# Performance work log

Hardware: AMD Instinct MI355X
Metric: run time of the kernel (lower is better)

The kernel has to match this reference:

```python
import jax, jax.numpy as jnp
import numpy as np


def _lstm_layer(xs, h0, c0, W, b):
    """Scan a single LSTM layer over time.
    xs: [T, B, D_in]; h0, c0: [B, H]; W: [D_in + H, 4H]; b: [4H].
    Returns (hs [T, B, H], h_last [B, H]).
    Gate math matches a standard flax LSTMCell: i, f, g, o gates,
    c' = sigmoid(f)*c + sigmoid(i)*tanh(g); h' = sigmoid(o)*tanh(c').
    """
    def step(carry, x_t):
        h, c = carry
        z = jnp.concatenate([x_t, h], axis=-1) @ W + b  # [B, 4H]
        i, f, g, o = jnp.split(z, 4, axis=-1)
        c_new = jax.nn.sigmoid(f) * c + jax.nn.sigmoid(i) * jnp.tanh(g)
        h_new = jax.nn.sigmoid(o) * jnp.tanh(c_new)
        return (h_new, c_new), h_new

    (h_last, _), hs = jax.lax.scan(step, (h0, c0), xs)
    return hs, h_last


def setup_inputs() -> dict:
    key = jax.random.key(0)
    ks = jax.random.split(key, 4)
    B, T, D_IN, H, L, OUT = 32, 512, 512, 1024, 4, 1024
    W_SCALE = 0.05  # keep gate pre-activations in a sane range
    x = jax.random.normal(ks[0], (B, T, D_IN), dtype=jnp.float32)
    h0 = jnp.zeros((L, B, H), dtype=jnp.float32)
    c0 = jnp.zeros((L, B, H), dtype=jnp.float32)
    W0 = jax.random.normal(ks[1], (D_IN + H, 4 * H), dtype=jnp.float32) * W_SCALE
    b0 = jnp.zeros((4 * H,), dtype=jnp.float32)
    Wl = jax.random.normal(ks[2], (L - 1, 2 * H, 4 * H), dtype=jnp.float32) * W_SCALE
    bl = jnp.zeros((L - 1, 4 * H), dtype=jnp.float32)
    Wout = jax.random.normal(ks[3], (H, OUT), dtype=jnp.float32) * W_SCALE
    bout = jnp.zeros((OUT,), dtype=jnp.float32)
    return {"x": x, "h0": h0, "c0": c0, "W0": W0, "b0": b0,
            "Wl": Wl, "bl": bl, "Wout": Wout, "bout": bout}


def reference(x, h0, c0, W0, b0, Wl, bl, Wout, bout):
    # x: [B, T, D_in] -> time-major for scan
    xs = jnp.transpose(x, (1, 0, 2))  # [T, B, D_in]
    hs, h_last = _lstm_layer(xs, h0[0], c0[0], W0, b0)
    n_deep = Wl.shape[0]  # small fixed layer count; Python loop is fine
    for l in range(n_deep):
        hs, h_last = _lstm_layer(hs, h0[l + 1], c0[l + 1], Wl[l], bl[l])
    # many-to-one: dense head on last layer's hidden at final timestep
    return h_last @ Wout + bout  # [B, output_size]
```

## Files before the change

### kernel.cpp

```cpp
#include <hip/hip_runtime.h>
#include <stdint.h>
#include <stddef.h>

typedef _Float16 half_t;
typedef __attribute__((ext_vector_type(8))) _Float16 f16x8;
typedef __attribute__((ext_vector_type(16))) float f32x16;
typedef unsigned long long u64;

#define TSEQ 512
#define NSTAGE 521
#define SLOT 32768
#define LSTRIDE ((size_t)513 * SLOT)

__device__ __forceinline__ float sigmoidf_(float x) { return 1.f / (1.f + __expf(-x)); }
__device__ __forceinline__ float tanhf_(float x) { return 1.f - 2.f / (__expf(2.f * x) + 1.f); }

__device__ __forceinline__ void async_copy16(const void* g, void* l) {
    __builtin_amdgcn_global_load_lds((const __attribute__((address_space(1))) void*)g,
                                     (__attribute__((address_space(3))) void*)l, 16, 0, 0);
}

__global__ void wconv_pack(const float* __restrict__ W0, const float* __restrict__ Wl,
                           half_t* __restrict__ WTp) {
    int idx = blockIdx.x * 256 + threadIdx.x;
    int lane = idx & 63, fi = (idx >> 6) & 31, wid = (idx >> 11) & 7;
    int lwg = idx >> 14;
    int cu = lwg & 63, l = lwg >> 6;
    int c = fi >> 1, half = fi & 1;
    int np = half * 32 + (lane & 31);
    int n = (np >> 4) * 1024 + cu * 16 + (np & 15);
    int kbase = wid * 256 + c * 16 + (lane >> 5) * 8;
    half_t tmp[8];
#pragma unroll
    for (int j = 0; j < 8; ++j) {
        int k = kbase + j;
        float v;
        if (l == 0) {
            if (k < 512) v = W0[(size_t)k * 4096 + n];
            else if (k < 1024) v = 0.f;
            else v = W0[(size_t)(k - 512) * 4096 + n];
        } else {
            v = Wl[((size_t)(l - 1) * 2048 + k) * 4096 + n];
        }
        tmp[j] = (half_t)v;
    }
    *(int4*)(WTp + (size_t)idx * 8) = *(int4*)tmp;
}

__global__ void xconv(const float* __restrict__ x, half_t* __restrict__ xb) {
    int idx = blockIdx.x * 256 + threadIdx.x;
    int b = idx & 31, c = (idx >> 5) & 127, t = idx >> 12;
    half_t tmp[8];
#pragma unroll
    for (int j = 0; j < 8; ++j)
        tmp[j] = (c < 64) ? (half_t)x[((size_t)b * 512 + t) * 512 + c * 8 + j] : (half_t)0.f;
    *(int4*)(xb + (size_t)idx * 8) = *(int4*)tmp;
}

__global__ void hinit(const float* __restrict__ h0, half_t* __restrict__ hO) {
    int idx = blockIdx.x * 256 + threadIdx.x;
    int b = idx & 31, c = (idx >> 5) & 127, l = idx >> 12;
    half_t tmp[8];
#pragma unroll
    for (int j = 0; j < 8; ++j) tmp[j] = (half_t)h0[(size_t)l * 32768 + b * 1024 + c * 8 + j];
    *(int4*)(hO + (size_t)l * LSTRIDE + (size_t)(c * 32 + b) * 8) = *(int4*)tmp;
}

__global__ void init_flags(int* f, int n) {
    int i = blockIdx.x * blockDim.x + threadIdx.x;
    if (i < n) f[i] = 0;
}

__global__ void __launch_bounds__(512, 2) lstm_pipe(
        const half_t* __restrict__ WTp, const half_t* __restrict__ xb,
        const float* __restrict__ b0, const float* __restrict__ bl,
        const float* __restrict__ c0, half_t* __restrict__ hO,
        int* __restrict__ flags) {
    __shared__ char smem[132096];
    float* zbuf = (float*)smem;
    half_t* hbuf = (half_t*)(smem + 131072);

    const int tid = threadIdx.x;
    const int wg = blockIdx.x;
    const int l = (wg & 7) >> 1;
    const int cu = ((wg >> 3) << 1) | (wg & 1);
    const int lwg = l * 64 + cu;
    const int lane = tid & 63, wid = tid >> 6;
    const bool skipq = (l == 0 && (wid >> 1) == 1);

    f16x8 bfr[32];
    {
        const char* wgw = (const char*)(WTp + (size_t)lwg * 131072);
#pragma unroll
        for (int it = 0; it < 16; ++it)
            async_copy16(wgw + it * 8192 + tid * 16, smem + it * 8192 + tid * 16);
        __syncthreads();
        if (wid < 4) {
#pragma unroll
            for (int c = 0; c < 32; ++c)
                bfr[c] = *(const f16x8*)(smem + (wid * 32 + c) * 1024 + lane * 16);
        }
        __syncthreads();
#pragma unroll
        for (int it = 0; it < 16; ++it)
            async_copy16(wgw + 131072 + it * 8192 + tid * 16, smem + it * 8192 + tid * 16);
        __syncthreads();
        if (wid >= 4) {
#pragma unroll
            for (int c = 0; c < 32; ++c)
                bfr[c] = *(const f16x8*)(smem + ((wid - 4) * 32 + c) * 1024 + lane * 16);
        }
        __syncthreads();
    }

    const int b = tid & 31, hc = tid >> 5;
    const int colg = cu * 16 + hc;
    const float* bias = (l == 0) ? b0 : (bl + (size_t)(l - 1) * 4096);
    const float bi = bias[colg], bf = bias[1024 + colg];
    const float bg = bias[2048 + colg], bo = bias[3072 + colg];
    float c_reg = c0[(size_t)l * 32768 + b * 1024 + colg];

    half_t* houtl = hO + (size_t)l * LSTRIDE;
    const half_t* hin_base = (l == 0) ? xb : (hO + (size_t)(l - 1) * LSTRIDE);

    const size_t aoff = (size_t)((wid & 3) * 32 + (lane >> 5)) * 256 + (size_t)(lane & 31) * 8;

    for (int s = 0; s < NSTAGE; ++s) {
        const int t = s - 3 * l;
        const bool active = (t >= 0 && t < TSEQ);
        const half_t* ap = nullptr;
        f16x8 ar[16];
        if (active && !skipq) {
            const half_t* srcx = (l == 0) ? (xb + (size_t)t * SLOT)
                                          : (hin_base + (size_t)(t + 1) * SLOT);
            const half_t* srch = houtl + (size_t)t * SLOT;
            ap = ((wid < 4) ? srcx : srch) + aoff;
            if (wid < 4) {
#pragma unroll
                for (int p = 0; p < 16; ++p) ar[p] = *(const f16x8*)(ap + (size_t)p * 512);
            }
        }
        if (tid < 64) {
            if (s >= 1) {
                const int* fp = &flags[(l * 64 + tid) * 16];
                while (__hip_atomic_load(fp, __ATOMIC_RELAXED, __HIP_MEMORY_SCOPE_AGENT) < s)
                    __builtin_amdgcn_s_sleep(1);
            }
        } else if (tid < 128 && l > 0 && s >= 2) {
            const int* fp = &flags[((l - 1) * 64 + (tid - 64)) * 16];
            while (__hip_atomic_load(fp, __ATOMIC_RELAXED, __HIP_MEMORY_SCOPE_AGENT) < s - 1)
                __builtin_amdgcn_s_sleep(2);
        }
        __syncthreads();
        if (active) {
            f32x16 acc0, acc1;
#pragma unroll
            for (int r = 0; r < 16; ++r) { acc0[r] = 0.f; acc1[r] = 0.f; }
            if (!skipq) {
                if (wid >= 4) {
#pragma unroll
                    for (int p = 0; p < 16; ++p) ar[p] = *(const f16x8*)(ap + (size_t)p * 512);
                }
#pragma unroll
                for (int c = 0; c < 16; ++c) {
                    acc0 = __builtin_amdgcn_mfma_f32_32x32x16_f16(ar[c], bfr[2 * c], acc0, 0, 0, 0);
                    acc1 = __builtin_amdgcn_mfma_f32_32x32x16_f16(ar[c], bfr[2 * c + 1], acc1, 0, 0, 0);
                }
            }
            {
                int colb = lane & 31;
                float* zc0 = zbuf + (size_t)colb * 257 + wid * 32 + 4 * (lane >> 5);
                float* zc1 = zbuf + (size_t)(32 + colb) * 257 + wid * 32 + 4 * (lane >> 5);
#pragma unroll
                for (int r = 0; r < 16; ++r) {
                    zc0[(r & 3) + 8 * (r >> 2)] = acc0[r];
                    zc1[(r & 3) + 8 * (r >> 2)] = acc1[r];
                }
            }
            __syncthreads();
            {
                float zg4[4];
#pragma unroll
                for (int gi = 0; gi < 4; ++gi) {
                    const float* zc = zbuf + (size_t)(gi * 16 + hc) * 257 + b;
                    zg4[gi] = ((zc[0] + zc[32]) + (zc[64] + zc[96]))
                            + ((zc[128] + zc[160]) + (zc[192] + zc[224]));
                }
                float zi = zg4[0] + bi, zf = zg4[1] + bf;
                float zg = zg4[2] + bg, zo = zg4[3] + bo;
                c_reg = sigmoidf_(zf) * c_reg + sigmoidf_(zi) * tanhf_(zg);
                float h = sigmoidf_(zo) * tanhf_(c_reg);
                hbuf[(hc >> 3) * 256 + b * 8 + (hc & 7)] = (half_t)h;
            }
            __syncthreads();
            if (tid < 128) {
                u64 v = ((const u64*)hbuf)[tid];
                u64* dst = (u64*)(houtl + (size_t)(t + 1) * SLOT) + (size_t)cu * 128 + tid;
                __hip_atomic_store(dst, v, __ATOMIC_RELAXED, __HIP_MEMORY_SCOPE_AGENT);
            }
        }
        __syncthreads();
        if (s < NSTAGE - 1 && tid == 0)
            __hip_atomic_store(&flags[lwg * 16], s + 1, __ATOMIC_RELAXED,
                               __HIP_MEMORY_SCOPE_AGENT);
    }
}

__global__ void head_gemm(const half_t* __restrict__ hO, const float* __restrict__ Wout,
                          const float* __restrict__ bout, float* __restrict__ out) {
    int o = blockIdx.x * 32 + (threadIdx.x & 31);
    int b = blockIdx.y * 8 + (threadIdx.x >> 5);
    const half_t* h = hO + (size_t)3 * LSTRIDE + (size_t)512 * SLOT + b * 8;
    float acc = 0.f;
    for (int kb = 0; kb < 128; ++kb) {
        const half_t* hp = h + (size_t)kb * 256;
#pragma unroll
        for (int j = 0; j < 8; ++j)
            acc += (float)hp[j] * Wout[(size_t)(kb * 8 + j) * 1024 + o];
    }
    out[b * 1024 + o] = acc + bout[o];
}

extern "C" void kernel_launch(void* const* d_in, const int* in_sizes, int n_in,
                              void* d_out, int out_size, void* d_ws, size_t ws_size,
                              hipStream_t stream) {
    const float* x    = (const float*)d_in[0];
    const float* h0   = (const float*)d_in[1];
    const float* c0   = (const float*)d_in[2];
    const float* W0   = (const float*)d_in[3];
    const float* b0   = (const float*)d_in[4];
    const float* Wl   = (const float*)d_in[5];
    const float* bl   = (const float*)d_in[6];
    const float* Wout = (const float*)d_in[7];
    const float* bout = (const float*)d_in[8];
    float* out = (float*)d_out;

    char* ws = (char*)d_ws;
    size_t off = 0;
    auto alloc = [&](size_t bytes) {
        size_t r = off;
        off = (off + bytes + 255) & ~(size_t)255;
        return r;
    };
    half_t* WTp = (half_t*)(ws + alloc((size_t)4 * 64 * 131072 * 2));
    half_t* xb  = (half_t*)(ws + alloc((size_t)512 * SLOT * 2));
    half_t* hO  = (half_t*)(ws + alloc((size_t)4 * LSTRIDE * 2));
    int* flags  = (int*)(ws + alloc((size_t)256 * 16 * 4));

    wconv_pack<<<16384, 256, 0, stream>>>(W0, Wl, WTp);
    xconv<<<8192, 256, 0, stream>>>(x, xb);
    hinit<<<64, 256, 0, stream>>>(h0, hO);
    init_flags<<<16, 256, 0, stream>>>(flags, 256 * 16);

    lstm_pipe<<<256, 512, 0, stream>>>(WTp, xb, b0, bl, c0, hO, flags);

    head_gemm<<<dim3(32, 4), 256, 0, stream>>>(hO, Wout, bout, out);
}
```

Before: 1.943 ms.

## Overlap input-projection MFMAs with flag spin-wait in persistent LSTM kernel

Waves 0-3, which handle the input-projection half (x or previous layer's h), now load their operands, run their MFMAs and write partial sums to LDS before the barrier. Waves 4 and 5 meanwhile spin on the same-layer and previous-layer flags. After the barrier, only the recurrent-half waves do their loads and MFMAs, so the critical path after synchronisation is shorter. The risk is a correctness hazard: the previous layer's h(t+1) is read by waves 0-3 before the previous-layer flag wait completes.

```diff
diff --git a/kernel.cpp b/kernel.cpp
--- a/kernel.cpp
+++ b/kernel.cpp
@@ -128,76 +128,92 @@
     for (int s = 0; s < NSTAGE; ++s) {
         const int t = s - 3 * l;
         const bool active = (t >= 0 && t < TSEQ);
-        const half_t* ap = nullptr;
-        f16x8 ar[16];
-        if (active && !skipq) {
-            const half_t* srcx = (l == 0) ? (xb + (size_t)t * SLOT)
-                                          : (hin_base + (size_t)(t + 1) * SLOT);
-            const half_t* srch = houtl + (size_t)t * SLOT;
-            ap = ((wid < 4) ? srcx : srch) + aoff;
-            if (wid < 4) {
-#pragma unroll
-                for (int p = 0; p < 16; ++p) ar[p] = *(const f16x8*)(ap + (size_t)p * 512);
-            }
-        }
-        if (tid < 64) {
+
+        if (wid < 4) {
+            if (active) {
+                f32x16 acc0, acc1;
+#pragma unroll
+                for (int r = 0; r < 16; ++r) { acc0[r] = 0.f; acc1[r] = 0.f; }
+                if (!skipq) {
+                    const half_t* ap = ((l == 0) ? (xb + (size_t)t * SLOT)
+                                                 : (hin_base + (size_t)(t + 1) * SLOT)) + aoff;
+                    f16x8 ar[16];
+#pragma unroll
+                    for (int p = 0; p < 16; ++p) ar[p] = *(const f16x8*)(ap + (size_t)p * 512);
+#pragma unroll
+                    for (int c = 0; c < 16; ++c) {
+                        acc0 = __builtin_amdgcn_mfma_f32_32x32x16_f16(ar[c], bfr[2 * c], acc0, 0, 0, 0);
+                        acc1 = __builtin_amdgcn_mfma_f32_32x32x16_f16(ar[c], bfr[2 * c + 1], acc1, 0, 0, 0);
+                    }
+                }
+                int colb = lane & 31;
+                float* zc0 = zbuf + (size_t)colb * 257 + wid * 32 + 4 * (lane >> 5);
+                float* zc1 = zbuf + (size_t)(32 + colb) * 257 + wid * 32 + 4 * (lane >> 5);
+#pragma unroll
+                for (int r = 0; r < 16; ++r) {
+                    zc0[(r & 3) + 8 * (r >> 2)] = acc0[r];
+                    zc1[(r & 3) + 8 * (r >> 2)] = acc1[r];
+                }
+            }
+        } else if (wid == 4) {
             if (s >= 1) {
-                const int* fp = &flags[(l * 64 + tid) * 16];
+                const int* fp = &flags[(l * 64 + lane) * 16];
                 while (__hip_atomic_load(fp, __ATOMIC_RELAXED, __HIP_MEMORY_SCOPE_AGENT) < s)
                     __builtin_amdgcn_s_sleep(1);
             }
-        } else if (tid < 128 && l > 0 && s >= 2) {
-            const int* fp = &flags[((l - 1) * 64 + (tid - 64)) * 16];
-            while (__hip_atomic_load(fp, __ATOMIC_RELAXED, __HIP_MEMORY_SCOPE_AGENT) < s - 1)
-                __builtin_amdgcn_s_sleep(2);
-        }
-        __syncthreads();
-        if (active) {
+        } else if (wid == 5) {
+            if (l > 0 && s >= 2) {
+                const int* fp = &flags[((l - 1) * 64 + lane) * 16];
+                while (__hip_atomic_load(fp, __ATOMIC_RELAXED, __HIP_MEMORY_SCOPE_AGENT) < s - 1)
+                    __builtin_amdgcn_s_sleep(2);
+            }
+        }
+        __syncthreads();
+
+        if (wid >= 4 && active) {
             f32x16 acc0, acc1;
 #pragma unroll
             for (int r = 0; r < 16; ++r) { acc0[r] = 0.f; acc1[r] = 0.f; }
-            if (!skipq) {
-                if (wid >= 4) {
-#pragma unroll
-                    for (int p = 0; p < 16; ++p) ar[p] = *(const f16x8*)(ap + (size_t)p * 512);
-                }
+            {
+                const half_t* ap = houtl + (size_t)t * SLOT + aoff;
+                f16x8 ar[16];
+#pragma unroll
+                for (int p = 0; p < 16; ++p) ar[p] = *(const f16x8*)(ap + (size_t)p * 512);
 #pragma unroll
                 for (int c = 0; c < 16; ++c) {
                     acc0 = __builtin_amdgcn_mfma_f32_32x32x16_f16(ar[c], bfr[2 * c], acc0, 0, 0, 0);
                     acc1 = __builtin_amdgcn_mfma_f32_32x32x16_f16(ar[c], bfr[2 * c + 1], acc1, 0, 0, 0);
                 }
             }
-            {
-                int colb = lane & 31;
-                float* zc0 = zbuf + (size_t)colb * 257 + wid * 32 + 4 * (lane >> 5);
-                float* zc1 = zbuf + (size_t)(32 + colb) * 257 + wid * 32 + 4 * (lane >> 5);
-#pragma unroll
-                for (int r = 0; r < 16; ++r) {
-                    zc0[(r & 3) + 8 * (r >> 2)] = acc0[r];
-                    zc1[(r & 3) + 8 * (r >> 2)] = acc1[r];
-                }
-            }
-            __syncthreads();
-            {
-                float zg4[4];
-#pragma unroll
-                for (int gi = 0; gi < 4; ++gi) {
-                    const float* zc = zbuf + (size_t)(gi * 16 + hc) * 257 + b;
-                    zg4[gi] = ((zc[0] + zc[32]) + (zc[64] + zc[96]))
-                            + ((zc[128] + zc[160]) + (zc[192] + zc[224]));
-                }
-                float zi = zg4[0] + bi, zf = zg4[1] + bf;
-                float zg = zg4[2] + bg, zo = zg4[3] + bo;
-                c_reg = sigmoidf_(zf) * c_reg + sigmoidf_(zi) * tanhf_(zg);
-                float h = sigmoidf_(zo) * tanhf_(c_reg);
-                hbuf[(hc >> 3) * 256 + b * 8 + (hc & 7)] = (half_t)h;
-            }
-            __syncthreads();
-            if (tid < 128) {
-                u64 v = ((const u64*)hbuf)[tid];
-                u64* dst = (u64*)(houtl + (size_t)(t + 1) * SLOT) + (size_t)cu * 128 + tid;
-                __hip_atomic_store(dst, v, __ATOMIC_RELAXED, __HIP_MEMORY_SCOPE_AGENT);
-            }
+            int colb = lane & 31;
+            float* zc0 = zbuf + (size_t)colb * 257 + wid * 32 + 4 * (lane >> 5);
+            float* zc1 = zbuf + (size_t)(32 + colb) * 257 + wid * 32 + 4 * (lane >> 5);
+#pragma unroll
+            for (int r = 0; r < 16; ++r) {
+                zc0[(r & 3) + 8 * (r >> 2)] = acc0[r];
+                zc1[(r & 3) + 8 * (r >> 2)] = acc1[r];
+            }
+        }
+        __syncthreads();
+        if (active) {
+            float zg4[4];
+#pragma unroll
+            for (int gi = 0; gi < 4; ++gi) {
+                const float* zc = zbuf + (size_t)(gi * 16 + hc) * 257 + b;
+                zg4[gi] = ((zc[0] + zc[32]) + (zc[64] + zc[96]))
+                        + ((zc[128] + zc[160]) + (zc[192] + zc[224]));
+            }
+            float zi = zg4[0] + bi, zf = zg4[1] + bf;
+            float zg = zg4[2] + bg, zo = zg4[3] + bo;
+            c_reg = sigmoidf_(zf) * c_reg + sigmoidf_(zi) * tanhf_(zg);
+            float h = sigmoidf_(zo) * tanhf_(c_reg);
+            hbuf[(hc >> 3) * 256 + b * 8 + (hc & 7)] = (half_t)h;
+        }
+        __syncthreads();
+        if (active && tid < 128) {
+            u64 v = ((const u64*)hbuf)[tid];
+            u64* dst = (u64*)(houtl + (size_t)(t + 1) * SLOT) + (size_t)cu * 128 + tid;
+            __hip_atomic_store(dst, v, __ATOMIC_RELAXED, __HIP_MEMORY_SCOPE_AGENT);
         }
         __syncthreads();
         if (s < NSTAGE - 1 && tid == 0)
```

Result: slower. 3.334 ms (+71.6%).
